# Optimization experiments

Measured on AMD Instinct MI355X. Metric: run time of the kernel, lower is better.

The kernel has to match this reference:

```python
import jax, jax.numpy as jnp
import numpy as np
import math

DIM = 768
HEADS = 8
DIM_HEAD = 64
INNER = HEADS * DIM_HEAD  # 512
B, L = 2, 4096
LN_EPS = 1e-5


def setup_inputs() -> dict:
    key = jax.random.key(0)
    ks = jax.random.split(key, 6)
    std = 0.02
    return {
        "x": jax.random.normal(ks[0], (B, L, DIM), dtype=jnp.float32),
        "ln_gamma": jnp.ones((DIM,), dtype=jnp.float32),
        "ln_beta": jnp.zeros((DIM,), dtype=jnp.float32),
        "Wq": jax.random.normal(ks[1], (DIM, INNER), dtype=jnp.float32) * std,
        "Wkv": jax.random.normal(ks[2], (DIM, 2 * INNER), dtype=jnp.float32) * std,
        "Wo": jax.random.normal(ks[3], (INNER, DIM), dtype=jnp.float32) * std,
    }


def reference(x, ln_gamma, ln_beta, Wq, Wkv, Wo):
    b, l, _ = x.shape
    # LayerNorm (eps=1e-5, affine)
    mu = jnp.mean(x, axis=-1, keepdims=True)
    var = jnp.mean(jnp.square(x - mu), axis=-1, keepdims=True)
    xn = (x - mu) * jax.lax.rsqrt(var + LN_EPS) * ln_gamma + ln_beta

    q = xn @ Wq                      # (b, l, inner)
    kv = xn @ Wkv                    # (b, l, 2*inner)
    k, v = jnp.split(kv, 2, axis=-1)

    def to_heads(t):
        return t.reshape(b, l, HEADS, DIM_HEAD).transpose(0, 2, 1, 3)  # (b,h,l,d)

    q, k, v = to_heads(q), to_heads(k), to_heads(v)

    scale = 1.0 / math.sqrt(math.sqrt(DIM_HEAD))
    # explicit quadratic scores, softmax in float32 as in original
    weight = jnp.einsum("bhid,bhjd->bhij", q * scale, k * scale)
    weight = jax.nn.softmax(weight.astype(jnp.float32), axis=-1).astype(q.dtype)
    out = jnp.einsum("bhij,bhjd->bhid", weight, v)       # (b,h,l,d)
    out = out.transpose(0, 2, 1, 3).reshape(b, l, INNER)  # merge heads
    return out @ Wo
```

## Files before the change

### kernel.cpp

```cpp
#include <hip/hip_runtime.h>
#include <hip/hip_bf16.h>


typedef __bf16 bf16_t;
typedef __bf16 bf16x4 __attribute__((ext_vector_type(4)));
typedef __bf16 bf16x8 __attribute__((ext_vector_type(8)));
typedef float f32x4 __attribute__((ext_vector_type(4)));

#define MFMA16(a, b, c) __builtin_amdgcn_mfma_f32_16x16x32_bf16((a), (b), (c), 0, 0, 0)

#define QSCALE 0.18033688011112042f

#define GLDS(gp, lp)                                                          \
    __builtin_amdgcn_global_load_lds(                                         \
        (const __attribute__((address_space(1))) void*)(gp),                  \
        (__attribute__((address_space(3))) void*)(lp), 16, 0, 0)

__device__ __forceinline__ int detect_f32(const unsigned int* __restrict__ xw) {
    const int l = threadIdx.x & 63;
    int cnt = 0;
#pragma unroll
    for (int j = 0; j < 2; ++j) {
        const unsigned int e = (xw[l * 2 + j] >> 7) & 0xFF;
        cnt += (e >= 100 && e <= 140) ? 1 : 0;
    }
#pragma unroll
    for (int off = 1; off < 64; off <<= 1) cnt += __shfl_xor(cnt, off, 64);
    return cnt < 64;
}

__global__ __launch_bounds__(256) void prep_kernel(
    const void* __restrict__ xv, const void* __restrict__ gv,
    const void* __restrict__ bv, const void* __restrict__ wq,
    const void* __restrict__ wkv, const void* __restrict__ wo,
    bf16_t* __restrict__ xn, bf16_t* __restrict__ WqkvT, bf16_t* __restrict__ WoT,
    int* __restrict__ flag) {
    const int f32 = detect_f32((const unsigned int*)xv);
    const int bid = blockIdx.x;
    const int t = threadIdx.x;
    if (bid == 0 && t == 0) *flag = f32;

    __shared__ bf16_t Ts[64 * 68];

    if (bid < 2048) {
        const int lane = t & 63;
        const int row = bid * 4 + (t >> 6);
        const int c0 = lane * 12;
        float v[12];
        if (f32) {
            const float* xr = (const float*)xv + (size_t)row * 768 + c0;
#pragma unroll
            for (int i = 0; i < 3; ++i) {
                const float4 q = *(const float4*)(xr + i * 4);
                v[i * 4] = q.x; v[i * 4 + 1] = q.y;
                v[i * 4 + 2] = q.z; v[i * 4 + 3] = q.w;
            }
        } else {
            const bf16_t* xr = (const bf16_t*)xv + (size_t)row * 768 + c0;
#pragma unroll
            for (int i = 0; i < 3; ++i) {
                const bf16x4 q = *(const bf16x4*)(xr + i * 4);
#pragma unroll
                for (int j = 0; j < 4; ++j) v[i * 4 + j] = (float)q[j];
            }
        }
        float s = 0.f, sq = 0.f;
#pragma unroll
        for (int j = 0; j < 12; ++j) { s += v[j]; sq += v[j] * v[j]; }
#pragma unroll
        for (int off = 1; off < 64; off <<= 1) {
            s += __shfl_xor(s, off, 64);
            sq += __shfl_xor(sq, off, 64);
        }
        const float mu = s * (1.0f / 768.0f);
        const float var = sq * (1.0f / 768.0f) - mu * mu;
        const float rstd = rsqrtf(var + 1e-5f);

        bf16_t* xo = xn + (size_t)row * 768 + c0;
#pragma unroll
        for (int i = 0; i < 3; ++i) {
            bf16x4 o;
#pragma unroll
            for (int j = 0; j < 4; ++j) {
                const int c = c0 + i * 4 + j;
                const float gc = f32 ? ((const float*)gv)[c] : (float)((const bf16_t*)gv)[c];
                const float bc = f32 ? ((const float*)bv)[c] : (float)((const bf16_t*)bv)[c];
                o[j] = (bf16_t)((v[i * 4 + j] - mu) * rstd * gc + bc);
            }
            *(bf16x4*)(xo + i * 4) = o;
        }
        return;
    }

    int idx = bid - 2048;
    const void* in;
    bf16_t* out;
    int R, C, cx, ry;
    if (idx < 96) {
        in = wq; out = WqkvT; R = 768; C = 512;
        cx = idx & 7; ry = idx >> 3;
    } else if (idx < 288) {
        idx -= 96;
        in = wkv; out = WqkvT + (size_t)512 * 768; R = 768; C = 1024;
        cx = idx & 15; ry = idx >> 4;
    } else {
        idx -= 288;
        in = wo; out = WoT; R = 512; C = 768;
        cx = idx % 12; ry = idx / 12;
    }
    const int r0 = ry * 64, c0 = cx * 64;
    {
        const int r = t >> 2, c = (t & 3) * 16;
        if (f32) {
            const float* src = (const float*)in + (size_t)(r0 + r) * C + c0 + c;
#pragma unroll
            for (int i = 0; i < 16; i += 4) {
                const float4 q = *(const float4*)(src + i);
                Ts[r * 68 + c + i] = (bf16_t)q.x;
                Ts[r * 68 + c + i + 1] = (bf16_t)q.y;
                Ts[r * 68 + c + i + 2] = (bf16_t)q.z;
                Ts[r * 68 + c + i + 3] = (bf16_t)q.w;
            }
        } else {
            const bf16_t* src = (const bf16_t*)in + (size_t)(r0 + r) * C + c0 + c;
            *(bf16x8*)&Ts[r * 68 + c] = *(const bf16x8*)src;
            *(bf16x8*)&Ts[r * 68 + c + 8] = *(const bf16x8*)(src + 8);
        }
    }
    __syncthreads();
    {
        const int oc = t >> 2, seg = (t & 3) * 16;
        bf16x8 v0, v1;
#pragma unroll
        for (int j = 0; j < 8; ++j) v0[j] = Ts[(seg + j) * 68 + oc];
#pragma unroll
        for (int j = 0; j < 8; ++j) v1[j] = Ts[(seg + 8 + j) * 68 + oc];
        bf16_t* dst = out + (size_t)(c0 + oc) * R + r0 + seg;
        *(bf16x8*)dst = v0;
        *(bf16x8*)(dst + 8) = v1;
    }
}

__global__ __launch_bounds__(256) void qkv_gemm(const bf16_t* __restrict__ A,
                                                const bf16_t* __restrict__ BT,
                                                bf16_t* __restrict__ qkv,
                                                bf16_t* __restrict__ vtg,
                                                int M, int N, int K) {
    const int m0 = blockIdx.y * 128;
    const int n0 = blockIdx.x * 128;
    __shared__ bf16_t As[128 * 32];
    __shared__ bf16_t Bs[128 * 32];

    const int t = threadIdx.x;
    const int lane = t & 63;
    const int w = t >> 6;
    const int wm = (w >> 1) * 64;
    const int wn = (w & 1) * 64;
    const int quad = lane >> 4;
    const int cl = lane & 15;

    f32x4 acc[4][4];
    const f32x4 z4 = {0.f, 0.f, 0.f, 0.f};
#pragma unroll
    for (int mi = 0; mi < 4; ++mi)
#pragma unroll
        for (int ni = 0; ni < 4; ++ni) acc[mi][ni] = z4;

    const int r0 = lane >> 2;
    const int c0 = (lane & 3) * 8;
    const bf16_t* AgL = A + (size_t)(m0 + w * 32 + r0) * K + c0;
    const bf16_t* AgH = A + (size_t)(m0 + w * 32 + 16 + r0) * K + c0;
    const bf16_t* BgL = BT + (size_t)(n0 + w * 32 + r0) * K + c0;
    const bf16_t* BgH = BT + (size_t)(n0 + w * 32 + 16 + r0) * K + c0;
    bf16_t* AdL = &As[(w * 32) * 32];
    bf16_t* AdH = &As[(w * 32 + 16) * 32];
    bf16_t* BdL = &Bs[(w * 32) * 32];
    bf16_t* BdH = &Bs[(w * 32 + 16) * 32];

    for (int kt = 0; kt < K; kt += 32) {
        __syncthreads();
        GLDS(AgL + kt, AdL);
        GLDS(AgH + kt, AdH);
        GLDS(BgL + kt, BdL);
        GLDS(BgH + kt, BdH);
        __syncthreads();

        const int ko = quad * 8;
        bf16x8 af[4], bfr[4];
#pragma unroll
        for (int mi = 0; mi < 4; ++mi)
            af[mi] = *(const bf16x8*)&As[(wm + mi * 16 + cl) * 32 + ko];
#pragma unroll
        for (int ni = 0; ni < 4; ++ni)
            bfr[ni] = *(const bf16x8*)&Bs[(wn + ni * 16 + cl) * 32 + ko];
#pragma unroll
        for (int mi = 0; mi < 4; ++mi)
#pragma unroll
            for (int ni = 0; ni < 4; ++ni)
                acc[mi][ni] = MFMA16(af[mi], bfr[ni], acc[mi][ni]);
    }

    if (n0 >= 1024) {
        const int b = m0 >> 12;
#pragma unroll
        for (int mi = 0; mi < 4; ++mi) {
#pragma unroll
            for (int ni = 0; ni < 4; ++ni) {
                const int tok = (m0 & 4095) + wm + mi * 16 + quad * 4;
                const int dl = n0 + wn + ni * 16 + cl - 1024;
                bf16x4 pk;
#pragma unroll
                for (int r4 = 0; r4 < 4; ++r4) pk[r4] = (bf16_t)acc[mi][ni][r4];
                *(bf16x4*)(vtg + ((size_t)(b * 8 + (dl >> 6)) * 64 + (dl & 63)) * 4096 +
                           tok) = pk;
            }
        }
    } else {
        const float sc = (n0 < 512) ? QSCALE : 1.0f;
#pragma unroll
        for (int mi = 0; mi < 4; ++mi) {
#pragma unroll
            for (int ni = 0; ni < 4; ++ni) {
#pragma unroll
                for (int r4 = 0; r4 < 4; ++r4) {
                    const int row = m0 + wm + mi * 16 + quad * 4 + r4;
                    const int col = n0 + wn + ni * 16 + cl;
                    qkv[(size_t)row * N + col] = (bf16_t)(acc[mi][ni][r4] * sc);
                }
            }
        }
    }
}

__global__ __launch_bounds__(128) void gemm_bt64(const bf16_t* __restrict__ A,
                                                 const bf16_t* __restrict__ BT,
                                                 void* __restrict__ C,
                                                 int M, int N, int K,
                                                 const int* __restrict__ out_flag) {
    const int m0 = blockIdx.y * 128;
    const int n0 = blockIdx.x * 64;
    __shared__ bf16_t As[128 * 32];
    __shared__ bf16_t Bs[64 * 32];

    const int t = threadIdx.x;
    const int lane = t & 63;
    const int w = t >> 6;
    const int quad = lane >> 4;
    const int cl = lane & 15;

    f32x4 acc[4][4];
    const f32x4 z4 = {0.f, 0.f, 0.f, 0.f};
#pragma unroll
    for (int mi = 0; mi < 4; ++mi)
#pragma unroll
        for (int ni = 0; ni < 4; ++ni) acc[mi][ni] = z4;

    const int r0 = lane >> 2;
    const int c0 = (lane & 3) * 8;
    const bf16_t* Ag = A + (size_t)(m0 + w * 64 + r0) * K + c0;
    const bf16_t* Bg = BT + (size_t)(n0 + w * 32 + r0) * K + c0;
    bf16_t* Ad = &As[(w * 64) * 32];
    bf16_t* Bd = &Bs[(w * 32) * 32];

    for (int kt = 0; kt < K; kt += 32) {
        __syncthreads();
#pragma unroll
        for (int i = 0; i < 4; ++i) GLDS(Ag + kt + (size_t)i * 16 * K, Ad + i * 512);
#pragma unroll
        for (int i = 0; i < 2; ++i) GLDS(Bg + kt + (size_t)i * 16 * K, Bd + i * 512);
        __syncthreads();

        const int ko = quad * 8;
        bf16x8 af[4], bfr[4];
#pragma unroll
        for (int mi = 0; mi < 4; ++mi)
            af[mi] = *(const bf16x8*)&As[(w * 64 + mi * 16 + cl) * 32 + ko];
#pragma unroll
        for (int ni = 0; ni < 4; ++ni)
            bfr[ni] = *(const bf16x8*)&Bs[(ni * 16 + cl) * 32 + ko];
#pragma unroll
        for (int mi = 0; mi < 4; ++mi)
#pragma unroll
            for (int ni = 0; ni < 4; ++ni)
                acc[mi][ni] = MFMA16(af[mi], bfr[ni], acc[mi][ni]);
    }

    const int f32out = *out_flag;
#pragma unroll
    for (int mi = 0; mi < 4; ++mi) {
#pragma unroll
        for (int ni = 0; ni < 4; ++ni) {
#pragma unroll
            for (int r4 = 0; r4 < 4; ++r4) {
                const int row = m0 + w * 64 + mi * 16 + quad * 4 + r4;
                const int col = n0 + ni * 16 + cl;
                if (f32out)
                    ((float*)C)[(size_t)row * N + col] = acc[mi][ni][r4];
                else
                    ((bf16_t*)C)[(size_t)row * N + col] = (bf16_t)acc[mi][ni][r4];
            }
        }
    }
}

__global__ __launch_bounds__(256, 2) void attn_kernel(const bf16_t* __restrict__ qkv,
                                                      const bf16_t* __restrict__ vtg,
                                                      bf16_t* __restrict__ ao) {
    const int qt = blockIdx.x;
    const int bh = blockIdx.y;
    const int b = bh >> 3, h = bh & 7;
    const int q0 = qt * 128;

    __shared__ bf16_t Ps[4][64 * 68];
    __shared__ bf16_t Ks[2][64 * 68];
    __shared__ bf16_t Vs[2][64 * 68];

    const int t = threadIdx.x;
    const int lane = t & 63;
    const int w = t >> 6;
    const int qsub = w & 1;
    const int kh = w >> 1;
    const int quad = lane >> 4;
    const int cl = lane & 15;

    const size_t rowbase = (size_t)b * 4096;
    const int qcol = h * 64;
    const int kcol = 512 + h * 64;

    bf16_t* Qtr = &Ps[0][0];
    {
        const bf16_t* qsrc = qkv + (rowbase + q0 + w * 32) * 1536 + qcol;
#pragma unroll
        for (int i = 0; i < 4; ++i)
            GLDS(qsrc + (size_t)(i * 8 + (lane >> 3)) * 1536 + (lane & 7) * 8,
                 Qtr + (w * 32 + i * 8) * 64);
    }
    __syncthreads();

    bf16x8 aq[4][2];
#pragma unroll
    for (int rt = 0; rt < 4; ++rt)
#pragma unroll
        for (int hh = 0; hh < 2; ++hh)
            aq[rt][hh] =
                *(const bf16x8*)&Qtr[(qsub * 64 + rt * 16 + cl) * 64 + hh * 32 + quad * 8];

    bf16x8 ones;
#pragma unroll
    for (int e = 0; e < 8; ++e) ones[e] = (bf16_t)1.0f;

    const f32x4 z4 = {0.f, 0.f, 0.f, 0.f};
    f32x4 o[4][4];
    f32x4 l_acc[4];
#pragma unroll
    for (int rt = 0; rt < 4; ++rt) {
        l_acc[rt] = z4;
#pragma unroll
        for (int ni = 0; ni < 4; ++ni) o[rt][ni] = z4;
    }

    const int t2 = qsub * 64 + lane;
    const int sr = t2 >> 1;
    const int sh = (t2 & 1) * 32;

    bf16x8 kreg[4], vreg[4];
    {
        const int k0 = kh * 2048;
        const bf16_t* ks = qkv + (rowbase + k0 + sr) * 1536 + kcol + sh;
        const bf16_t* vs = vtg + ((size_t)bh * 64 + sr) * 4096 + k0 + sh;
#pragma unroll
        for (int o8 = 0; o8 < 4; ++o8) {
            kreg[o8] = *(const bf16x8*)(ks + o8 * 8);
            vreg[o8] = *(const bf16x8*)(vs + o8 * 8);
        }
    }

    for (int it = 0; it < 32; ++it) {
        __syncthreads();
#pragma unroll
        for (int o8 = 0; o8 < 4; ++o8) {
            *(bf16x8*)&Ks[kh][sr * 68 + sh + o8 * 8] = kreg[o8];
            *(bf16x8*)&Vs[kh][sr * 68 + sh + o8 * 8] = vreg[o8];
        }
        __syncthreads();

        if (it < 31) {
            const int k0n = kh * 2048 + (it + 1) * 64;
            const bf16_t* ks = qkv + (rowbase + k0n + sr) * 1536 + kcol + sh;
            const bf16_t* vs = vtg + ((size_t)bh * 64 + sr) * 4096 + k0n + sh;
#pragma unroll
            for (int o8 = 0; o8 < 4; ++o8) {
                kreg[o8] = *(const bf16x8*)(ks + o8 * 8);
                vreg[o8] = *(const bf16x8*)(vs + o8 * 8);
            }
        }

        const int ko = quad * 8;
        bf16x8 kb[4][2];
#pragma unroll
        for (int ni = 0; ni < 4; ++ni) {
            kb[ni][0] = *(const bf16x8*)&Ks[kh][(ni * 16 + cl) * 68 + ko];
            kb[ni][1] = *(const bf16x8*)&Ks[kh][(ni * 16 + cl) * 68 + 32 + ko];
        }
#pragma unroll
        for (int rt = 0; rt < 4; ++rt) {
#pragma unroll
            for (int ni = 0; ni < 4; ++ni) {
                f32x4 s = z4;
                s = MFMA16(kb[ni][0], aq[rt][0], s);
                s = MFMA16(kb[ni][1], aq[rt][1], s);
                bf16x4 pk;
#pragma unroll
                for (int r4 = 0; r4 < 4; ++r4) pk[r4] = (bf16_t)exp2f(s[r4]);
                *(bf16x4*)&Ps[w][(rt * 16 + cl) * 68 + ni * 16 + quad * 4] = pk;
            }
        }

        bf16x8 vb[4][2];
#pragma unroll
        for (int ni = 0; ni < 4; ++ni) {
            vb[ni][0] = *(const bf16x8*)&Vs[kh][(ni * 16 + cl) * 68 + ko];
            vb[ni][1] = *(const bf16x8*)&Vs[kh][(ni * 16 + cl) * 68 + 32 + ko];
        }
#pragma unroll
        for (int rt = 0; rt < 4; ++rt) {
            const bf16x8 p0 = *(const bf16x8*)&Ps[w][(rt * 16 + cl) * 68 + ko];
            const bf16x8 p1 = *(const bf16x8*)&Ps[w][(rt * 16 + cl) * 68 + 32 + ko];
#pragma unroll
            for (int ni = 0; ni < 4; ++ni) {
                o[rt][ni] = MFMA16(p0, vb[ni][0], o[rt][ni]);
                o[rt][ni] = MFMA16(p1, vb[ni][1], o[rt][ni]);
            }
            l_acc[rt] = MFMA16(p0, ones, l_acc[rt]);
            l_acc[rt] = MFMA16(p1, ones, l_acc[rt]);
        }
    }

    float* cb = (float*)&Ps[0][0];
    __syncthreads();
    if (kh == 1) {
#pragma unroll
        for (int rt = 0; rt < 4; ++rt) {
#pragma unroll
            for (int r4 = 0; r4 < 4; ++r4) {
                const int row = rt * 16 + quad * 4 + r4;
                float* rp = cb + qsub * 4160 + row * 65;
#pragma unroll
                for (int ni = 0; ni < 4; ++ni) rp[ni * 16 + cl] = o[rt][ni][r4];
                if (cl == 0) rp[64] = l_acc[rt][r4];
            }
        }
    }
    __syncthreads();
    if (kh == 0) {
#pragma unroll
        for (int rt = 0; rt < 4; ++rt) {
#pragma unroll
            for (int r4 = 0; r4 < 4; ++r4) {
                const int row = rt * 16 + quad * 4 + r4;
                const float* rp = cb + qsub * 4160 + row * 65;
                const float inv = 1.0f / (l_acc[rt][r4] + rp[64]);
                const size_t orow = rowbase + q0 + qsub * 64 + row;
#pragma unroll
                for (int ni = 0; ni < 4; ++ni)
                    ao[orow * 512 + h * 64 + ni * 16 + cl] =
                        (bf16_t)((o[rt][ni][r4] + rp[ni * 16 + cl]) * inv);
            }
        }
    }
}

extern "C" void kernel_launch(void* const* d_in, const int* in_sizes, int n_in,
                              void* d_out, int out_size, void* d_ws, size_t ws_size,
                              hipStream_t stream) {
    const void* x = d_in[0];
    const void* gamma = d_in[1];
    const void* beta = d_in[2];
    const void* Wq = d_in[3];
    const void* Wkv = d_in[4];
    const void* Wo = d_in[5];

    char* wsb = (char*)d_ws;
    int* flag = (int*)wsb;
    bf16_t* xn = (bf16_t*)(wsb + 256);
    bf16_t* WqkvT = xn + (size_t)8192 * 768;
    bf16_t* WoT = WqkvT + (size_t)1536 * 768;
    bf16_t* qkv = WoT + (size_t)768 * 512;
    bf16_t* aob = xn;
    bf16_t* vtg = (bf16_t*)d_out;

    prep_kernel<<<2432, 256, 0, stream>>>(x, gamma, beta, Wq, Wkv, Wo, xn, WqkvT, WoT,
                                          flag);

    qkv_gemm<<<dim3(12, 64), 256, 0, stream>>>(xn, WqkvT, qkv, vtg, 8192, 1536, 768);

    attn_kernel<<<dim3(32, 16), 256, 0, stream>>>(qkv, vtg, aob);

    gemm_bt64<<<dim3(12, 64), 128, 0, stream>>>(aob, WoT, d_out, 8192, 768, 512, flag);
}
```

Before: 256.6 us.

## Rewrite attention inner loop with 32x32 MFMA and register-resident P

Restructures the attention kernel so each wave owns 32 query rows across the full key range using 32x32x16 bf16 MFMAs. This removes the split-K halves and their LDS reduction. Probabilities are converted and rearranged in registers with permlane32_swap instead of being staged through LDS. K and V tiles are double-buffered via direct global-to-LDS loads with an XOR swizzle instead of padded rows, and s_setprio is set around the MFMA blocks. In exchange the loop runs twice as many iterations per block and relies on the swizzle being bank-conflict free.

```diff
diff --git a/kernel.cpp b/kernel.cpp
--- a/kernel.cpp
+++ b/kernel.cpp
@@ -6,8 +6,12 @@
 typedef __bf16 bf16x4 __attribute__((ext_vector_type(4)));
 typedef __bf16 bf16x8 __attribute__((ext_vector_type(8)));
 typedef float f32x4 __attribute__((ext_vector_type(4)));
+typedef float f32x16 __attribute__((ext_vector_type(16)));
+typedef unsigned int u32x2 __attribute__((ext_vector_type(2)));
+typedef unsigned int u32x4 __attribute__((ext_vector_type(4)));
 
 #define MFMA16(a, b, c) __builtin_amdgcn_mfma_f32_16x16x32_bf16((a), (b), (c), 0, 0, 0)
+#define MFMA32(a, b, c) __builtin_amdgcn_mfma_f32_32x32x16_bf16((a), (b), (c), 0, 0, 0)
 
 #define QSCALE 0.18033688011112042f
 
@@ -308,164 +312,133 @@
                                                       bf16_t* __restrict__ ao) {
     const int qt = blockIdx.x;
     const int bh = blockIdx.y;
-    const int b = bh >> 3, h = bh & 7;
-    const int q0 = qt * 128;
-
-    __shared__ bf16_t Ps[4][64 * 68];
-    __shared__ bf16_t Ks[2][64 * 68];
-    __shared__ bf16_t Vs[2][64 * 68];
+    const int b = bh >> 3, hd = bh & 7;
+
+    __shared__ bf16_t Ks[2][64 * 64];
+    __shared__ bf16_t Vs[2][64 * 64];
 
     const int t = threadIdx.x;
     const int lane = t & 63;
     const int w = t >> 6;
-    const int qsub = w & 1;
-    const int kh = w >> 1;
-    const int quad = lane >> 4;
-    const int cl = lane & 15;
+    const int c = lane & 31;
+    const int h = lane >> 5;
 
     const size_t rowbase = (size_t)b * 4096;
-    const int qcol = h * 64;
-    const int kcol = 512 + h * 64;
-
-    bf16_t* Qtr = &Ps[0][0];
+    const int qcol = hd * 64;
+    const int kcol = 512 + hd * 64;
+    const int q0w = qt * 128 + w * 32;
+
+    bf16x8 qf[4];
     {
-        const bf16_t* qsrc = qkv + (rowbase + q0 + w * 32) * 1536 + qcol;
-#pragma unroll
-        for (int i = 0; i < 4; ++i)
-            GLDS(qsrc + (size_t)(i * 8 + (lane >> 3)) * 1536 + (lane & 7) * 8,
-                 Qtr + (w * 32 + i * 8) * 64);
-    }
-    __syncthreads();
-
-    bf16x8 aq[4][2];
-#pragma unroll
-    for (int rt = 0; rt < 4; ++rt)
-#pragma unroll
-        for (int hh = 0; hh < 2; ++hh)
-            aq[rt][hh] =
-                *(const bf16x8*)&Qtr[(qsub * 64 + rt * 16 + cl) * 64 + hh * 32 + quad * 8];
+        const bf16_t* qp = qkv + (rowbase + q0w + c) * 1536 + qcol + h * 8;
+#pragma unroll
+        for (int ks = 0; ks < 4; ++ks) qf[ks] = *(const bf16x8*)(qp + ks * 16);
+    }
 
     bf16x8 ones;
 #pragma unroll
     for (int e = 0; e < 8; ++e) ones[e] = (bf16_t)1.0f;
 
-    const f32x4 z4 = {0.f, 0.f, 0.f, 0.f};
-    f32x4 o[4][4];
-    f32x4 l_acc[4];
-#pragma unroll
-    for (int rt = 0; rt < 4; ++rt) {
-        l_acc[rt] = z4;
-#pragma unroll
-        for (int ni = 0; ni < 4; ++ni) o[rt][ni] = z4;
-    }
-
-    const int t2 = qsub * 64 + lane;
-    const int sr = t2 >> 1;
-    const int sh = (t2 & 1) * 32;
-
-    bf16x8 kreg[4], vreg[4];
-    {
-        const int k0 = kh * 2048;
-        const bf16_t* ks = qkv + (rowbase + k0 + sr) * 1536 + kcol + sh;
-        const bf16_t* vs = vtg + ((size_t)bh * 64 + sr) * 4096 + k0 + sh;
-#pragma unroll
-        for (int o8 = 0; o8 < 4; ++o8) {
-            kreg[o8] = *(const bf16x8*)(ks + o8 * 8);
-            vreg[o8] = *(const bf16x8*)(vs + o8 * 8);
-        }
-    }
-
-    for (int it = 0; it < 32; ++it) {
+    f32x16 z16, o0, o1, l_acc;
+#pragma unroll
+    for (int i = 0; i < 16; ++i) z16[i] = 0.f;
+    o0 = z16; o1 = z16; l_acc = z16;
+
+    const int sr = t >> 3;
+    const int seg = t & 7;
+    const int swz = (seg ^ (sr & 7)) * 8;
+    const bf16_t* kgp = qkv + (rowbase + sr) * 1536 + kcol + swz;
+    const bf16_t* vgp = vtg + ((size_t)bh * 64 + sr) * 4096 + swz;
+
+    int ksw[4];
+#pragma unroll
+    for (int ks = 0; ks < 4; ++ks) ksw[ks] = ((2 * ks + h) ^ (c & 7)) * 8;
+
+    GLDS(kgp, &Ks[0][w * 512]);
+    GLDS(kgp + (size_t)32 * 1536, &Ks[0][2048 + w * 512]);
+    GLDS(vgp, &Vs[0][w * 512]);
+    GLDS(vgp + (size_t)32 * 4096, &Vs[0][2048 + w * 512]);
+
+    for (int it = 0; it < 64; ++it) {
+        const int cur = it & 1;
         __syncthreads();
-#pragma unroll
-        for (int o8 = 0; o8 < 4; ++o8) {
-            *(bf16x8*)&Ks[kh][sr * 68 + sh + o8 * 8] = kreg[o8];
-            *(bf16x8*)&Vs[kh][sr * 68 + sh + o8 * 8] = vreg[o8];
-        }
-        __syncthreads();
-
-        if (it < 31) {
-            const int k0n = kh * 2048 + (it + 1) * 64;
-            const bf16_t* ks = qkv + (rowbase + k0n + sr) * 1536 + kcol + sh;
-            const bf16_t* vs = vtg + ((size_t)bh * 64 + sr) * 4096 + k0n + sh;
-#pragma unroll
-            for (int o8 = 0; o8 < 4; ++o8) {
-                kreg[o8] = *(const bf16x8*)(ks + o8 * 8);
-                vreg[o8] = *(const bf16x8*)(vs + o8 * 8);
-            }
-        }
-
-        const int ko = quad * 8;
-        bf16x8 kb[4][2];
-#pragma unroll
-        for (int ni = 0; ni < 4; ++ni) {
-            kb[ni][0] = *(const bf16x8*)&Ks[kh][(ni * 16 + cl) * 68 + ko];
-            kb[ni][1] = *(const bf16x8*)&Ks[kh][(ni * 16 + cl) * 68 + 32 + ko];
-        }
-#pragma unroll
-        for (int rt = 0; rt < 4; ++rt) {
-#pragma unroll
-            for (int ni = 0; ni < 4; ++ni) {
-                f32x4 s = z4;
-                s = MFMA16(kb[ni][0], aq[rt][0], s);
-                s = MFMA16(kb[ni][1], aq[rt][1], s);
-                bf16x4 pk;
-#pragma unroll
-                for (int r4 = 0; r4 < 4; ++r4) pk[r4] = (bf16_t)exp2f(s[r4]);
-                *(bf16x4*)&Ps[w][(rt * 16 + cl) * 68 + ni * 16 + quad * 4] = pk;
-            }
-        }
-
-        bf16x8 vb[4][2];
-#pragma unroll
-        for (int ni = 0; ni < 4; ++ni) {
-            vb[ni][0] = *(const bf16x8*)&Vs[kh][(ni * 16 + cl) * 68 + ko];
-            vb[ni][1] = *(const bf16x8*)&Vs[kh][(ni * 16 + cl) * 68 + 32 + ko];
-        }
-#pragma unroll
-        for (int rt = 0; rt < 4; ++rt) {
-            const bf16x8 p0 = *(const bf16x8*)&Ps[w][(rt * 16 + cl) * 68 + ko];
-            const bf16x8 p1 = *(const bf16x8*)&Ps[w][(rt * 16 + cl) * 68 + 32 + ko];
-#pragma unroll
-            for (int ni = 0; ni < 4; ++ni) {
-                o[rt][ni] = MFMA16(p0, vb[ni][0], o[rt][ni]);
-                o[rt][ni] = MFMA16(p1, vb[ni][1], o[rt][ni]);
-            }
-            l_acc[rt] = MFMA16(p0, ones, l_acc[rt]);
-            l_acc[rt] = MFMA16(p1, ones, l_acc[rt]);
-        }
-    }
-
-    float* cb = (float*)&Ps[0][0];
-    __syncthreads();
-    if (kh == 1) {
-#pragma unroll
-        for (int rt = 0; rt < 4; ++rt) {
-#pragma unroll
-            for (int r4 = 0; r4 < 4; ++r4) {
-                const int row = rt * 16 + quad * 4 + r4;
-                float* rp = cb + qsub * 4160 + row * 65;
-#pragma unroll
-                for (int ni = 0; ni < 4; ++ni) rp[ni * 16 + cl] = o[rt][ni][r4];
-                if (cl == 0) rp[64] = l_acc[rt][r4];
-            }
-        }
-    }
-    __syncthreads();
-    if (kh == 0) {
-#pragma unroll
-        for (int rt = 0; rt < 4; ++rt) {
-#pragma unroll
-            for (int r4 = 0; r4 < 4; ++r4) {
-                const int row = rt * 16 + quad * 4 + r4;
-                const float* rp = cb + qsub * 4160 + row * 65;
-                const float inv = 1.0f / (l_acc[rt][r4] + rp[64]);
-                const size_t orow = rowbase + q0 + qsub * 64 + row;
-#pragma unroll
-                for (int ni = 0; ni < 4; ++ni)
-                    ao[orow * 512 + h * 64 + ni * 16 + cl] =
-                        (bf16_t)((o[rt][ni][r4] + rp[ni * 16 + cl]) * inv);
-            }
+
+        if (it < 63) {
+            const size_t gofs = (size_t)(it + 1) * 64;
+            GLDS(kgp + gofs * 1536, &Ks[cur ^ 1][w * 512]);
+            GLDS(kgp + (gofs + 32) * 1536, &Ks[cur ^ 1][2048 + w * 512]);
+            GLDS(vgp + gofs, &Vs[cur ^ 1][w * 512]);
+            GLDS(vgp + (size_t)32 * 4096 + gofs, &Vs[cur ^ 1][2048 + w * 512]);
+        }
+
+        __builtin_amdgcn_s_setprio(1);
+        f32x16 s0, s1;
+        {
+            const bf16x8 k0 = *(const bf16x8*)&Ks[cur][c * 64 + ksw[0]];
+            const bf16x8 k1 = *(const bf16x8*)&Ks[cur][(32 + c) * 64 + ksw[0]];
+            s0 = MFMA32(k0, qf[0], z16);
+            s1 = MFMA32(k1, qf[0], z16);
+        }
+#pragma unroll
+        for (int ks = 1; ks < 4; ++ks) {
+            const bf16x8 k0 = *(const bf16x8*)&Ks[cur][c * 64 + ksw[ks]];
+            const bf16x8 k1 = *(const bf16x8*)&Ks[cur][(32 + c) * 64 + ksw[ks]];
+            s0 = MFMA32(k0, qf[ks], s0);
+            s1 = MFMA32(k1, qf[ks], s1);
+        }
+        __builtin_amdgcn_s_setprio(0);
+
+        bf16x8 pf[4];
+#pragma unroll
+        for (int tt = 0; tt < 2; ++tt) {
+            const f32x16 sv = tt ? s1 : s0;
+            float ex[16];
+#pragma unroll
+            for (int i = 0; i < 16; ++i) ex[i] = exp2f(sv[i]);
+            unsigned int pk[4][2];
+#pragma unroll
+            for (int g = 0; g < 4; ++g) {
+                asm("v_cvt_pk_bf16_f32 %0, %1, %2"
+                    : "=v"(pk[g][0]) : "v"(ex[4 * g + 0]), "v"(ex[4 * g + 1]));
+                asm("v_cvt_pk_bf16_f32 %0, %1, %2"
+                    : "=v"(pk[g][1]) : "v"(ex[4 * g + 2]), "v"(ex[4 * g + 3]));
+            }
+#pragma unroll
+            for (int k2 = 0; k2 < 2; ++k2) {
+                u32x4 fu;
+#pragma unroll
+                for (int cc = 0; cc < 2; ++cc) {
+                    const u32x2 r = __builtin_amdgcn_permlane32_swap(
+                        pk[2 * k2][cc], pk[2 * k2 + 1][cc], false, false);
+                    fu[cc] = r[0];
+                    fu[2 + cc] = r[1];
+                }
+                pf[tt * 2 + k2] = __builtin_bit_cast(bf16x8, fu);
+            }
+        }
+
+        __builtin_amdgcn_s_setprio(1);
+#pragma unroll
+        for (int ks = 0; ks < 4; ++ks) {
+            const bf16x8 v0 = *(const bf16x8*)&Vs[cur][c * 64 + ksw[ks]];
+            const bf16x8 v1 = *(const bf16x8*)&Vs[cur][(32 + c) * 64 + ksw[ks]];
+            o0 = MFMA32(pf[ks], v0, o0);
+            o1 = MFMA32(pf[ks], v1, o1);
+            l_acc = MFMA32(pf[ks], ones, l_acc);
+        }
+        __builtin_amdgcn_s_setprio(0);
+    }
+
+#pragma unroll
+    for (int g = 0; g < 4; ++g) {
+#pragma unroll
+        for (int r4 = 0; r4 < 4; ++r4) {
+            const int reg = 4 * g + r4;
+            const int row = r4 + 8 * g + 4 * h;
+            const float inv = 1.0f / l_acc[reg];
+            bf16_t* op = ao + (rowbase + q0w + row) * 512 + qcol;
+            op[c] = (bf16_t)(o0[reg] * inv);
+            op[32 + c] = (bf16_t)(o1[reg] * inv);
         }
     }
 }
```

Measured after the change: 266.0 us. 3.7% more time.

## Double-buffer K/V tiles in LDS and interleave per-row-tile softmax with PV

Applied to the files above, without the earlier changes.

The attention kernel now keeps two LDS buffers for the K and V tiles, unrolled by two. This halves the block barriers per KV tile and lets the store of the next tile overlap compute on the current one. The P scratch shrinks to a 16-row tile per wave and is consumed right after each row tile's exp, which frees LDS for the double buffer. Exp uses the raw amdgcn exp2 builtin with packed bf16 conversion via inline asm, and MFMA sections get raised wave priority. LDS use grows overall, which could limit the two-blocks-per-CU occupancy, and the cross-wave hazards on the reused P buffer now depend on program order within each wave.

```diff
diff --git a/kernel.cpp b/kernel.cpp
--- a/kernel.cpp
+++ b/kernel.cpp
@@ -6,6 +6,7 @@
 typedef __bf16 bf16x4 __attribute__((ext_vector_type(4)));
 typedef __bf16 bf16x8 __attribute__((ext_vector_type(8)));
 typedef float f32x4 __attribute__((ext_vector_type(4)));
+typedef unsigned int u32x2 __attribute__((ext_vector_type(2)));
 
 #define MFMA16(a, b, c) __builtin_amdgcn_mfma_f32_16x16x32_bf16((a), (b), (c), 0, 0, 0)
 
@@ -311,9 +312,9 @@
     const int b = bh >> 3, h = bh & 7;
     const int q0 = qt * 128;
 
-    __shared__ bf16_t Ps[4][64 * 68];
-    __shared__ bf16_t Ks[2][64 * 68];
-    __shared__ bf16_t Vs[2][64 * 68];
+    __shared__ bf16_t Ps[4][16 * 68];
+    __shared__ bf16_t Ks[2][2][64 * 68];
+    __shared__ bf16_t Vs[2][2][64 * 68];
 
     const int t = threadIdx.x;
     const int lane = t & 63;
@@ -327,7 +328,7 @@
     const int qcol = h * 64;
     const int kcol = 512 + h * 64;
 
-    bf16_t* Qtr = &Ps[0][0];
+    bf16_t* Qtr = &Ks[0][0][0];
     {
         const bf16_t* qsrc = qkv + (rowbase + q0 + w * 32) * 1536 + qcol;
 #pragma unroll
@@ -335,6 +336,35 @@
             GLDS(qsrc + (size_t)(i * 8 + (lane >> 3)) * 1536 + (lane & 7) * 8,
                  Qtr + (w * 32 + i * 8) * 64);
     }
+
+    const int t2 = qsub * 64 + lane;
+    const int sr = t2 >> 1;
+    const int sh = (t2 & 1) * 32;
+    const bf16_t* kgp = qkv + (rowbase + kh * 2048 + sr) * 1536 + kcol + sh;
+    const bf16_t* vgp = vtg + ((size_t)bh * 64 + sr) * 4096 + kh * 2048 + sh;
+    size_t koff = 0, voff = 0;
+    bf16x8 kreg[4], vreg[4];
+
+#define LOADT()                                                       \
+    do {                                                              \
+        _Pragma("unroll")                                             \
+        for (int o8 = 0; o8 < 4; ++o8) {                              \
+            kreg[o8] = *(const bf16x8*)(kgp + koff + o8 * 8);         \
+            vreg[o8] = *(const bf16x8*)(vgp + voff + o8 * 8);         \
+        }                                                             \
+        koff += (size_t)64 * 1536;                                    \
+        voff += 64;                                                   \
+    } while (0)
+#define STORET(bq)                                                    \
+    do {                                                              \
+        _Pragma("unroll")                                             \
+        for (int o8 = 0; o8 < 4; ++o8) {                              \
+            *(bf16x8*)&Ks[bq][kh][sr * 68 + sh + o8 * 8] = kreg[o8];  \
+            *(bf16x8*)&Vs[bq][kh][sr * 68 + sh + o8 * 8] = vreg[o8];  \
+        }                                                             \
+    } while (0)
+
+    LOADT();
     __syncthreads();
 
     bf16x8 aq[4][2];
@@ -345,6 +375,11 @@
             aq[rt][hh] =
                 *(const bf16x8*)&Qtr[(qsub * 64 + rt * 16 + cl) * 64 + hh * 32 + quad * 8];
 
+    __syncthreads();
+    STORET(0);
+    LOADT();
+    __syncthreads();
+
     bf16x8 ones;
 #pragma unroll
     for (int e = 0; e < 8; ++e) ones[e] = (bf16_t)1.0f;
@@ -359,85 +394,66 @@
         for (int ni = 0; ni < 4; ++ni) o[rt][ni] = z4;
     }
 
-    const int t2 = qsub * 64 + lane;
-    const int sr = t2 >> 1;
-    const int sh = (t2 & 1) * 32;
-
-    bf16x8 kreg[4], vreg[4];
-    {
-        const int k0 = kh * 2048;
-        const bf16_t* ks = qkv + (rowbase + k0 + sr) * 1536 + kcol + sh;
-        const bf16_t* vs = vtg + ((size_t)bh * 64 + sr) * 4096 + k0 + sh;
-#pragma unroll
-        for (int o8 = 0; o8 < 4; ++o8) {
-            kreg[o8] = *(const bf16x8*)(ks + o8 * 8);
-            vreg[o8] = *(const bf16x8*)(vs + o8 * 8);
-        }
-    }
-
-    for (int it = 0; it < 32; ++it) {
+    const int ko = quad * 8;
+
+#define COMPUTE(bq)                                                              \
+    do {                                                                         \
+        bf16x8 kb[4][2], vb[4][2];                                               \
+        _Pragma("unroll")                                                        \
+        for (int ni = 0; ni < 4; ++ni) {                                         \
+            kb[ni][0] = *(const bf16x8*)&Ks[bq][kh][(ni * 16 + cl) * 68 + ko];   \
+            kb[ni][1] = *(const bf16x8*)&Ks[bq][kh][(ni * 16 + cl) * 68 + 32 + ko]; \
+            vb[ni][0] = *(const bf16x8*)&Vs[bq][kh][(ni * 16 + cl) * 68 + ko];   \
+            vb[ni][1] = *(const bf16x8*)&Vs[bq][kh][(ni * 16 + cl) * 68 + 32 + ko]; \
+        }                                                                        \
+        __builtin_amdgcn_s_setprio(1);                                           \
+        _Pragma("unroll")                                                        \
+        for (int rt = 0; rt < 4; ++rt) {                                         \
+            _Pragma("unroll")                                                    \
+            for (int ni = 0; ni < 4; ++ni) {                                     \
+                f32x4 s = z4;                                                    \
+                s = MFMA16(kb[ni][0], aq[rt][0], s);                             \
+                s = MFMA16(kb[ni][1], aq[rt][1], s);                             \
+                const float e0 = __builtin_amdgcn_exp2f(s[0]);                   \
+                const float e1 = __builtin_amdgcn_exp2f(s[1]);                   \
+                const float e2 = __builtin_amdgcn_exp2f(s[2]);                   \
+                const float e3 = __builtin_amdgcn_exp2f(s[3]);                   \
+                u32x2 pk;                                                        \
+                asm("v_cvt_pk_bf16_f32 %0, %1, %2" : "=v"(pk[0]) : "v"(e0), "v"(e1)); \
+                asm("v_cvt_pk_bf16_f32 %0, %1, %2" : "=v"(pk[1]) : "v"(e2), "v"(e3)); \
+                *(u32x2*)&Ps[w][cl * 68 + ni * 16 + quad * 4] = pk;              \
+            }                                                                    \
+            const bf16x8 p0 = *(const bf16x8*)&Ps[w][cl * 68 + ko];              \
+            const bf16x8 p1 = *(const bf16x8*)&Ps[w][cl * 68 + 32 + ko];         \
+            _Pragma("unroll")                                                    \
+            for (int ni = 0; ni < 4; ++ni) {                                     \
+                o[rt][ni] = MFMA16(p0, vb[ni][0], o[rt][ni]);                    \
+                o[rt][ni] = MFMA16(p1, vb[ni][1], o[rt][ni]);                    \
+            }                                                                    \
+            l_acc[rt] = MFMA16(p0, ones, l_acc[rt]);                             \
+            l_acc[rt] = MFMA16(p1, ones, l_acc[rt]);                             \
+        }                                                                        \
+        __builtin_amdgcn_s_setprio(0);                                           \
+    } while (0)
+
+    for (int it2 = 0; it2 < 16; ++it2) {
+        STORET(1);
+        if (it2 < 15) LOADT();
+        COMPUTE(0);
         __syncthreads();
-#pragma unroll
-        for (int o8 = 0; o8 < 4; ++o8) {
-            *(bf16x8*)&Ks[kh][sr * 68 + sh + o8 * 8] = kreg[o8];
-            *(bf16x8*)&Vs[kh][sr * 68 + sh + o8 * 8] = vreg[o8];
-        }
+
+        if (it2 < 15) {
+            STORET(0);
+            LOADT();
+        }
+        COMPUTE(1);
         __syncthreads();
-
-        if (it < 31) {
-            const int k0n = kh * 2048 + (it + 1) * 64;
-            const bf16_t* ks = qkv + (rowbase + k0n + sr) * 1536 + kcol + sh;
-            const bf16_t* vs = vtg + ((size_t)bh * 64 + sr) * 4096 + k0n + sh;
-#pragma unroll
-            for (int o8 = 0; o8 < 4; ++o8) {
-                kreg[o8] = *(const bf16x8*)(ks + o8 * 8);
-                vreg[o8] = *(const bf16x8*)(vs + o8 * 8);
-            }
-        }
-
-        const int ko = quad * 8;
-        bf16x8 kb[4][2];
-#pragma unroll
-        for (int ni = 0; ni < 4; ++ni) {
-            kb[ni][0] = *(const bf16x8*)&Ks[kh][(ni * 16 + cl) * 68 + ko];
-            kb[ni][1] = *(const bf16x8*)&Ks[kh][(ni * 16 + cl) * 68 + 32 + ko];
-        }
-#pragma unroll
-        for (int rt = 0; rt < 4; ++rt) {
-#pragma unroll
-            for (int ni = 0; ni < 4; ++ni) {
-                f32x4 s = z4;
-                s = MFMA16(kb[ni][0], aq[rt][0], s);
-                s = MFMA16(kb[ni][1], aq[rt][1], s);
-                bf16x4 pk;
-#pragma unroll
-                for (int r4 = 0; r4 < 4; ++r4) pk[r4] = (bf16_t)exp2f(s[r4]);
-                *(bf16x4*)&Ps[w][(rt * 16 + cl) * 68 + ni * 16 + quad * 4] = pk;
-            }
-        }
-
-        bf16x8 vb[4][2];
-#pragma unroll
-        for (int ni = 0; ni < 4; ++ni) {
-            vb[ni][0] = *(const bf16x8*)&Vs[kh][(ni * 16 + cl) * 68 + ko];
-            vb[ni][1] = *(const bf16x8*)&Vs[kh][(ni * 16 + cl) * 68 + 32 + ko];
-        }
-#pragma unroll
-        for (int rt = 0; rt < 4; ++rt) {
-            const bf16x8 p0 = *(const bf16x8*)&Ps[w][(rt * 16 + cl) * 68 + ko];
-            const bf16x8 p1 = *(const bf16x8*)&Ps[w][(rt * 16 + cl) * 68 + 32 + ko];
-#pragma unroll
-            for (int ni = 0; ni < 4; ++ni) {
-                o[rt][ni] = MFMA16(p0, vb[ni][0], o[rt][ni]);
-                o[rt][ni] = MFMA16(p1, vb[ni][1], o[rt][ni]);
-            }
-            l_acc[rt] = MFMA16(p0, ones, l_acc[rt]);
-            l_acc[rt] = MFMA16(p1, ones, l_acc[rt]);
-        }
-    }
-
-    float* cb = (float*)&Ps[0][0];
-    __syncthreads();
+    }
+#undef LOADT
+#undef STORET
+#undef COMPUTE
+
+    float* cb = (float*)&Ks[0][0][0];
     if (kh == 1) {
 #pragma unroll
         for (int rt = 0; rt < 4; ++rt) {
```

Result: faster. 234.1 us (-8.8%).
